# Optimization experiments

Hardware: AMD Instinct MI355X
Metric: run time of the kernel (lower is better)

## Reference

```python
import jax, jax.numpy as jnp
import numpy as np

SOFTCAP = 15.0
EPS_RMS = 1e-6
EPS_L2 = 1e-12


def rms_norm(x):
    # F.rms_norm without affine weight
    return x * jax.lax.rsqrt(jnp.mean(x * x, axis=-1, keepdims=True) + EPS_RMS)


def l2_normalize(x):
    # F.normalize(dim=-1): x / max(||x||, eps)
    n = jnp.sqrt(jnp.sum(x * x, axis=-1, keepdims=True))
    return x / jnp.maximum(n, EPS_L2)


def setup_inputs() -> dict:
    key = jax.random.key(0)
    ks = jax.random.split(key, 7)
    B, D, H, KVH, HD = 2, 1024, 16, 4, 64
    chunk_start_idx, chunk_len, n_scratchpad = 2048, 2048, 64
    T = chunk_start_idx + chunk_len + n_scratchpad  # 4160
    s = 0.02
    return {
        "x": jax.random.normal(ks[0], (B, T, D), dtype=jnp.float32),
        "Wq": jax.random.normal(ks[1], (D, D), dtype=jnp.float32) * s,
        "Wk": jax.random.normal(ks[2], (KVH * HD, D), dtype=jnp.float32) * s,
        "Wv": jax.random.normal(ks[3], (KVH * HD, D), dtype=jnp.float32) * s,
        "Wo": jax.random.normal(ks[4], (D, D), dtype=jnp.float32) * s,
        "Wfc": jax.random.normal(ks[5], (4 * D, D), dtype=jnp.float32) * s,
        "Wproj": jax.random.normal(ks[6], (D, 4 * D), dtype=jnp.float32) * s,
        "chunk_start_idx": chunk_start_idx,
        "chunk_len": chunk_len,
        "n_scratchpad": n_scratchpad,
    }


def reference(x, Wq, Wk, Wv, Wo, Wfc, Wproj, chunk_start_idx, chunk_len, n_scratchpad):
    B, T, D = x.shape
    H = 16
    KVH = Wk.shape[0] // (D // H)
    HD = D // H
    update_start = chunk_start_idx
    n_update = T - update_start

    x_norm = rms_norm(x)
    x_upd = x_norm[:, update_start:]

    q = (x_upd @ Wq.T).reshape(B, n_update, H, HD).transpose(0, 2, 1, 3)   # [B,H,Q,hd]
    k = (x_norm @ Wk.T).reshape(B, T, KVH, HD).transpose(0, 2, 1, 3)       # [B,KVH,T,hd]
    v = (x_norm @ Wv.T).reshape(B, T, KVH, HD).transpose(0, 2, 1, 3)

    q = l2_normalize(q)
    k = l2_normalize(k)

    if KVH < H:
        rep = H // KVH
        k = jnp.repeat(k, rep, axis=1)
        v = jnp.repeat(v, rep, axis=1)

    scale = 1.0 / jnp.sqrt(jnp.float32(HD))
    scores = jnp.einsum("bhqd,bhkd->bhqk", q, k) * scale
    q_pos = jnp.arange(update_start, T)[:, None]
    kv_pos = jnp.arange(T)[None, :]
    mask = kv_pos <= q_pos  # [Q,T] causal
    scores = jnp.where(mask[None, None], scores, -jnp.inf)
    probs = jax.nn.softmax(scores, axis=-1)
    attn = jnp.einsum("bhqk,bhkd->bhqd", probs, v)             # [B,H,Q,hd]
    attn = attn.transpose(0, 2, 1, 3).reshape(B, n_update, D)

    attn_out = attn @ Wo.T
    attn_out = SOFTCAP * jnp.tanh(attn_out / SOFTCAP)

    x_new = x[:, update_start:] + attn_out
    h = rms_norm(x_new) @ Wfc.T
    h = jnp.square(jax.nn.relu(h))  # nanochat MLP: relu(x)^2
    x_new = x_new + h @ Wproj.T

    if update_start > 0:
        return jnp.concatenate([x[:, :update_start], x_new], axis=1)
    return x_new
```

## Files before the change

kernel.cpp:

```cpp
#include <hip/hip_runtime.h>
#include <hip/hip_bf16.h>

#define B_   2
#define T_   4160
#define D_   1024
#define H_   16
#define KVH_ 4
#define HD_  64
#define UPD  2048
#define NU   2112
#define MQ   (B_*NU)
#define MT   (B_*T_)

typedef unsigned short u16;
typedef unsigned int u32;
typedef __attribute__((ext_vector_type(8))) short bf16x8;
typedef __attribute__((ext_vector_type(4))) float f32x4;
typedef __attribute__((ext_vector_type(4))) unsigned short u16x4;

__device__ __forceinline__ float bf2f(u16 u){ return __uint_as_float(((unsigned)u)<<16); }
__device__ __forceinline__ u16 f2bf(float f){
  unsigned u = __float_as_uint(f);
  u += 0x7FFF + ((u>>16)&1);
  return (u16)(u>>16);
}

__device__ __forceinline__ void gll16(const void* g, void* l){
  __builtin_amdgcn_global_load_lds((const __attribute__((address_space(1))) char*)g,
                                   (__attribute__((address_space(3))) char*)l, 16, 0, 0);
}

__global__ void cast_bf16(const float* __restrict__ in, u16* __restrict__ o, int n){
  int i = blockIdx.x*blockDim.x + threadIdx.x;
  if (i*4 < n){
    float4 v = ((const float4*)in)[i];
    u16x4 u; u.x=f2bf(v.x); u.y=f2bf(v.y); u.z=f2bf(v.z); u.w=f2bf(v.w);
    ((u16x4*)o)[i] = u;
  }
}

__global__ void rmsnorm_kernel(const float* __restrict__ in, u16* __restrict__ obf,
                               float* __restrict__ copy_out, int withcopy){
  int row = blockIdx.x;
  int t = threadIdx.x;
  const float* xr = in + (size_t)row*D_;
  float4 v = ((const float4*)xr)[t];
  float ss = v.x*v.x + v.y*v.y + v.z*v.z + v.w*v.w;
  #pragma unroll
  for (int o=32;o;o>>=1) ss += __shfl_xor(ss, o);
  __shared__ float red[4];
  if ((t&63)==0) red[t>>6] = ss;
  __syncthreads();
  float tot = red[0]+red[1]+red[2]+red[3];
  float sc = rsqrtf(tot*(1.0f/D_) + 1e-6f);
  u16x4 o4; o4.x=f2bf(v.x*sc); o4.y=f2bf(v.y*sc); o4.z=f2bf(v.z*sc); o4.w=f2bf(v.w*sc);
  ((u16x4*)(obf + (size_t)row*D_))[t] = o4;
  if (withcopy && (row % T_) < UPD)
    ((float4*)(copy_out + (size_t)row*D_))[t] = v;
}

__global__ void l2norm_kernel(u16* __restrict__ buf, int nvec){
  int vid = blockIdx.x*4 + (threadIdx.x>>6);
  int ln = threadIdx.x & 63;
  if (vid >= nvec) return;
  u16* p = buf + (size_t)vid*64 + ln;
  float x = bf2f(*p);
  float ss = x*x;
  #pragma unroll
  for (int o=32;o;o>>=1) ss += __shfl_xor(ss, o);
  float n = sqrtf(ss);
  n = (n < 1e-12f) ? 1e-12f : n;
  *p = f2bf(x / n);
}

template<int EPI, int AMAP, int BN>
__global__ __launch_bounds__(256) void gemm_bt(
    const u16* __restrict__ A, const u16* __restrict__ Bw, void* __restrict__ C,
    void* __restrict__ aux, int M, int N, int K)
{
  constexpr int MI = (BN==128) ? 4 : 2;
  __shared__ alignas(16) u16 sA[2][4096];
  __shared__ alignas(16) u16 sB[2][BN*32];
  unsigned nwg = gridDim.x*gridDim.y;
  unsigned flat = blockIdx.y*gridDim.x + blockIdx.x;
  unsigned nf = (flat&7)*(nwg>>3) + (flat>>3);
  int m0 = (int)(nf / gridDim.x) * 128;
  int n0 = (int)(nf % gridDim.x) * BN;
  int tid = threadIdx.x;
  int wv = tid>>6, ln = tid&63;
  int wr = (BN==128) ? (wv>>1) : wv;
  int wc = (BN==128) ? (wv&1)  : 0;
  int lr = ln&15, lg = ln>>4;

  auto stage = [&](int bu, int kt){
    #pragma unroll
    for (int c=0;c<2;c++){
      int ci = c*256 + tid;
      int row = ci>>2, colb = (ci&3)*16;
      int arow = m0 + row;
      if (AMAP==1) arow = (arow/NU)*T_ + UPD + (arow%NU);
      const u16* src = A + (size_t)arow*K + kt*32 + (colb>>1);
      gll16(src, (char*)sA[bu] + (c*256 + wv*64)*16);
    }
    #pragma unroll
    for (int c=0;c<BN/64;c++){
      int ci = c*256 + tid;
      int row = ci>>2, colb = (ci&3)*16;
      const u16* src = Bw + (size_t)(n0+row)*K + kt*32 + (colb>>1);
      gll16(src, (char*)sB[bu] + (c*256 + wv*64)*16);
    }
  };

  f32x4 acc[MI][4] = {};
  int nk = K>>5;
  stage(0,0);
  __syncthreads();
  for (int kt=0; kt<nk; ++kt){
    int bu = kt&1;
    if (kt+1<nk) stage(bu^1, kt+1);
    bf16x8 af[MI], bfr[4];
    #pragma unroll
    for (int i=0;i<MI;i++)
      af[i]  = *(const bf16x8*)&sA[bu][(wr*(MI*16) + i*16 + lr)*32 + lg*8];
    #pragma unroll
    for (int j=0;j<4;j++)
      bfr[j] = *(const bf16x8*)&sB[bu][(wc*64 + j*16 + lr)*32 + lg*8];
    #pragma unroll
    for (int i=0;i<MI;i++)
      #pragma unroll
      for (int j=0;j<4;j++)
        acc[i][j] = __builtin_amdgcn_mfma_f32_16x16x32_bf16(af[i], bfr[j], acc[i][j], 0,0,0);
    __syncthreads();
  }
  #pragma unroll
  for (int i=0;i<MI;i++)
    #pragma unroll
    for (int j=0;j<4;j++){
      int grow0 = m0 + wr*(MI*16) + i*16 + lg*4;
      int gcol  = n0 + wc*64 + j*16 + lr;
      if (EPI==5){
        if (gcol < 256){
          #pragma unroll
          for (int r=0;r<4;r++)
            ((u16*)C)[(size_t)(grow0+r)*256 + gcol] = f2bf(acc[i][j][r]);
        } else {
          int bb = grow0 / T_;
          int t  = grow0 - bb*T_;
          int kvh = (gcol>>6)&3, d = gcol&63;
          u16x4 pk;
          #pragma unroll
          for (int r=0;r<4;r++) pk[r] = f2bf(acc[i][j][r]);
          *(u16x4*)((u16*)aux + ((size_t)((bb*KVH_+kvh)*64 + d))*T_ + t) = pk;
        }
      } else {
        #pragma unroll
        for (int r=0;r<4;r++){
          int grow = grow0 + r;
          float cv = acc[i][j][r];
          if (EPI==0){
            ((u16*)C)[(size_t)grow*N + gcol] = f2bf(cv);
          } else if (EPI==1){
            int b = grow/NU, t = grow - b*NU;
            float e = __expf(cv*(2.0f/15.0f));
            float val = 15.f*(e-1.f)/(e+1.f) + ((const float*)aux)[((size_t)(b*T_ + UPD + t))*D_ + gcol];
            ((float*)C)[(size_t)grow*N + gcol] = val;
          } else if (EPI==2){
            float rr = cv>0.f ? cv : 0.f;
            ((u16*)C)[(size_t)grow*N + gcol] = f2bf(rr*rr);
          } else {
            int b = grow/NU, t = grow - b*NU;
            float val = ((const float*)aux)[(size_t)grow*N + gcol] + cv;
            ((float*)C)[((size_t)(b*T_ + UPD + t))*D_ + gcol] = val;
          }
        }
      }
    }
}

template<bool DIAG>
__device__ __forceinline__ void sm_pack(const f32x4 (&s)[2][4], char* spw,
                                        int lr, int lg, int ktb, int qbg){
  #pragma unroll
  for (int qi=0;qi<2;qi++)
    #pragma unroll
    for (int k2=0;k2<4;k2++){
      float p[4];
      #pragma unroll
      for (int r=0;r<4;r++){
        float pv = __builtin_amdgcn_exp2f(s[qi][k2][r]*0.18033688f);
        if (DIAG){
          int kpos = ktb + k2*16 + lg*4 + r;
          int qpos = qbg + qi*16 + lr;
          if (kpos > qpos) pv = 0.f;
        }
        p[r] = pv;
      }
      __hip_bfloat162 w0 = __float22bfloat162_rn(float2{p[0],p[1]});
      __hip_bfloat162 w1 = __float22bfloat162_rn(float2{p[2],p[3]});
      uint2 wd; wd.x = *(u32*)&w0; wd.y = *(u32*)&w1;
      *(uint2*)(spw + (qi*16+lr)*128 + ((k2*32 + lg*8) ^ ((lr&7)<<4))) = wd;
    }
}

__global__ __launch_bounds__(256) void attn_kernel(
    const u16* __restrict__ qb, const u16* __restrict__ kb,
    const u16* __restrict__ vT, u16* __restrict__ ab)
{
  __shared__ alignas(16) u16 sK[2][64*64];
  __shared__ alignas(16) u16 sV[2][64*64];
  __shared__ alignas(16) u16 sP[4][32*64];
  unsigned flat = (blockIdx.z*4u + blockIdx.y)*66u + blockIdx.x;
  unsigned nf = (flat&7)*66u + (flat>>3);
  int qi_blk = 65 - (int)(nf % 66u);
  unsigned khb = nf / 66u;
  int kh = (int)(khb & 3), b = (int)(khb >> 2);
  int tid = threadIdx.x, wv = tid>>6, ln = tid&63;
  int lr = ln&15, lg = ln>>4;
  int h = kh*4 + wv;
  int qrow0 = qi_blk*32;
  int qbg = UPD + qrow0;
  char* spw = (char*)&sP[wv][0];

  bf16x8 qf[2][2];
  #pragma unroll
  for (int qi=0;qi<2;qi++){
    const u16* qp = qb + (size_t)(b*NU + qrow0 + qi*16 + lr)*D_ + h*HD_;
    qf[qi][0] = *(const bf16x8*)(qp + lg*8);
    qf[qi][1] = *(const bf16x8*)(qp + 32 + lg*8);
  }
  bf16x8 ones;
  #pragma unroll
  for (int i=0;i<8;i++) ones[i] = (short)0x3F80;

  f32x4 accO[2][4] = {};
  f32x4 accD[2] = {};

  auto stage = [&](int bu, int kt){
    #pragma unroll
    for (int cc=0; cc<2; ++cc){
      int ci = cc*256 + tid;
      int row = ci>>3, slotb = (ci&7)*16;
      int scolb = slotb ^ ((row&7)<<4);
      gll16(kb + (size_t)(b*T_ + kt*64 + row)*256 + kh*HD_ + (scolb>>1),
            (char*)sK[bu] + (cc*256 + wv*64)*16);
    }
    #pragma unroll
    for (int cc=0; cc<2; ++cc){
      int ci = cc*256 + tid;
      int row = ci>>3, slotb = (ci&7)*16;
      int scolb = slotb ^ ((row&7)<<4);
      gll16(vT + (size_t)((b*KVH_+kh)*64 + row)*T_ + kt*64 + (scolb>>1),
            (char*)sV[bu] + (cc*256 + wv*64)*16);
    }
  };

  int nkt = 33 + (qi_blk>>1);
  stage(0,0);
  __syncthreads();
  for (int kt=0; kt<nkt; ++kt){
    int bu = kt&1;
    if (kt+1 < nkt) stage(bu^1, kt+1);
    f32x4 s[2][4];
    #pragma unroll
    for (int qi=0;qi<2;qi++)
      #pragma unroll
      for (int k2=0;k2<4;k2++) s[qi][k2] = (f32x4){0.f,0.f,0.f,0.f};
    #pragma unroll
    for (int k2=0;k2<4;k2++){
      int row = k2*16 + lr;
      int sw = (row&7)<<4;
      bf16x8 k0 = *(const bf16x8*)((const char*)sK[bu] + row*128 + ((lg*16)^sw));
      bf16x8 k1 = *(const bf16x8*)((const char*)sK[bu] + row*128 + ((64+lg*16)^sw));
      #pragma unroll
      for (int qi=0;qi<2;qi++){
        s[qi][k2] = __builtin_amdgcn_mfma_f32_16x16x32_bf16(k0, qf[qi][0], s[qi][k2], 0,0,0);
        s[qi][k2] = __builtin_amdgcn_mfma_f32_16x16x32_bf16(k1, qf[qi][1], s[qi][k2], 0,0,0);
      }
    }
    if (kt+1 < nkt) sm_pack<false>(s, spw, lr, lg, kt*64, qbg);
    else            sm_pack<true >(s, spw, lr, lg, kt*64, qbg);
    bf16x8 pf[2][2];
    #pragma unroll
    for (int qi=0;qi<2;qi++)
      #pragma unroll
      for (int hf=0;hf<2;hf++)
        pf[qi][hf] = *(const bf16x8*)(spw + (qi*16+lr)*128 + ((hf*64 + lg*16) ^ ((lr&7)<<4)));
    #pragma unroll
    for (int dt=0; dt<4; ++dt){
      int row = dt*16 + lr;
      int sw = (row&7)<<4;
      bf16x8 v0 = *(const bf16x8*)((const char*)sV[bu] + row*128 + ((lg*16)^sw));
      bf16x8 v1 = *(const bf16x8*)((const char*)sV[bu] + row*128 + ((64+lg*16)^sw));
      #pragma unroll
      for (int qi=0;qi<2;qi++){
        accO[qi][dt] = __builtin_amdgcn_mfma_f32_16x16x32_bf16(pf[qi][0], v0, accO[qi][dt], 0,0,0);
        accO[qi][dt] = __builtin_amdgcn_mfma_f32_16x16x32_bf16(pf[qi][1], v1, accO[qi][dt], 0,0,0);
      }
    }
    #pragma unroll
    for (int qi=0;qi<2;qi++){
      accD[qi] = __builtin_amdgcn_mfma_f32_16x16x32_bf16(pf[qi][0], ones, accD[qi], 0,0,0);
      accD[qi] = __builtin_amdgcn_mfma_f32_16x16x32_bf16(pf[qi][1], ones, accD[qi], 0,0,0);
    }
    __syncthreads();
  }
  #pragma unroll
  for (int qi=0;qi<2;qi++)
    #pragma unroll
    for (int dt=0; dt<4; ++dt)
      #pragma unroll
      for (int r=0;r<4;r++){
        float val = accO[qi][dt][r] / accD[qi][r];
        size_t row = (size_t)(b*NU + qrow0 + qi*16 + lg*4 + r);
        ab[row*D_ + h*HD_ + dt*16 + lr] = f2bf(val);
      }
}

extern "C" void kernel_launch(void* const* d_in, const int* in_sizes, int n_in,
                              void* d_out, int out_size, void* d_ws, size_t ws_size,
                              hipStream_t stream)
{
  const float* x     = (const float*)d_in[0];
  const float* Wq    = (const float*)d_in[1];
  const float* Wk    = (const float*)d_in[2];
  const float* Wv    = (const float*)d_in[3];
  const float* Wo    = (const float*)d_in[4];
  const float* Wfc   = (const float*)d_in[5];
  const float* Wproj = (const float*)d_in[6];
  float* out = (float*)d_out;

  char* ws = (char*)d_ws;
  size_t off = 0;
  auto alloc = [&](size_t bytes)->char*{ char* p = ws + off; off += (bytes + 255) & ~(size_t)255; return p; };
  u16* wqb  = (u16*)alloc((size_t)D_*D_*2);
  u16* wkvb = (u16*)alloc((size_t)512*D_*2);
  u16* wob  = (u16*)alloc((size_t)D_*D_*2);
  u16* wfcb = (u16*)alloc((size_t)4096*D_*2);
  u16* wpb  = (u16*)alloc((size_t)D_*4096*2);
  u16* xn   = (u16*)alloc((size_t)MT*D_*2);
  u16* qB   = (u16*)alloc((size_t)MQ*D_*2);
  u16* kB   = (u16*)alloc((size_t)MT*256*2);
  u16* vTb  = (u16*)alloc((size_t)B_*KVH_*64*T_*2);
  u16* aB   = (u16*)alloc((size_t)MQ*D_*2);
  float* xnew = (float*)alloc((size_t)MQ*D_*4);
  u16* xn2  = (u16*)alloc((size_t)MQ*D_*2);
  u16* hB   = (u16*)alloc((size_t)MQ*4096*2);
  (void)ws_size; (void)in_sizes; (void)n_in; (void)out_size;

  cast_bf16<<<1024, 256, 0, stream>>>(Wq, wqb, D_*D_);
  cast_bf16<<<256,  256, 0, stream>>>(Wk, wkvb, 256*D_);
  cast_bf16<<<256,  256, 0, stream>>>(Wv, wkvb + (size_t)256*D_, 256*D_);
  cast_bf16<<<1024, 256, 0, stream>>>(Wo, wob, D_*D_);
  cast_bf16<<<4096, 256, 0, stream>>>(Wfc, wfcb, 4096*D_);
  cast_bf16<<<4096, 256, 0, stream>>>(Wproj, wpb, D_*4096);

  rmsnorm_kernel<<<MT, 256, 0, stream>>>(x, xn, out, 1);

  gemm_bt<0,1,64><<<dim3(16,33), 256, 0, stream>>>(xn, wqb, qB, nullptr, MQ, D_,  D_);
  gemm_bt<5,0,64><<<dim3(8,65),  256, 0, stream>>>(xn, wkvb, kB, vTb, MT, 512, D_);

  l2norm_kernel<<<(MQ*H_)/4, 256, 0, stream>>>(qB, MQ*H_);
  l2norm_kernel<<<(MT*KVH_)/4, 256, 0, stream>>>(kB, MT*KVH_);

  attn_kernel<<<dim3(66,4,2), 256, 0, stream>>>(qB, kB, vTb, aB);

  gemm_bt<1,0,64><<<dim3(16,33), 256, 0, stream>>>(aB, wob, xnew, (void*)x, MQ, D_, D_);

  rmsnorm_kernel<<<MQ, 256, 0, stream>>>(xnew, xn2, nullptr, 0);
  gemm_bt<2,0,128><<<dim3(32,33), 256, 0, stream>>>(xn2, wfcb, hB, nullptr, MQ, 4096, D_);
  gemm_bt<3,0,64><<<dim3(16,33), 256, 0, stream>>>(hB, wpb, out, xnew, MQ, D_, 4096);
}
```

Baseline: 445.2 us.

## Triple-buffer GEMM and attention loads with vmcnt waits, fuse weight casts

GEMM and attention kernels move from double to triple-buffered LDS staging. Each iteration waits on a partial vmcnt and issues one barrier instead of a full __syncthreads, so loads two tiles ahead overlap compute. Load addresses are precomputed, and the GEMM LDS layout gets an XOR swizzle to reduce bank conflicts. The six weight casts become one launch, and the softmax scale folds into the K l2norm, dropping a multiply in the attention exp. The costs are more LDS per block, which may lower occupancy, and relying on hand-placed waitcnt counts for correctness.

Measured after the change: 454.6 us. 2.1% more time.

```diff
diff --git a/kernel.cpp b/kernel.cpp
--- a/kernel.cpp
+++ b/kernel.cpp
@@ -30,13 +30,29 @@
                                    (__attribute__((address_space(3))) char*)l, 16, 0, 0);
 }
 
-__global__ void cast_bf16(const float* __restrict__ in, u16* __restrict__ o, int n){
-  int i = blockIdx.x*blockDim.x + threadIdx.x;
-  if (i*4 < n){
-    float4 v = ((const float4*)in)[i];
-    u16x4 u; u.x=f2bf(v.x); u.y=f2bf(v.y); u.z=f2bf(v.z); u.w=f2bf(v.w);
-    ((u16x4*)o)[i] = u;
-  }
+template<int N> __device__ __forceinline__ void wait_vm(){
+  if constexpr(N==0) asm volatile("s_waitcnt vmcnt(0)" ::: "memory");
+  else if constexpr(N==3) asm volatile("s_waitcnt vmcnt(3)" ::: "memory");
+  else if constexpr(N==4) asm volatile("s_waitcnt vmcnt(4)" ::: "memory");
+}
+
+__global__ void cast_all(const float* __restrict__ s0, const float* __restrict__ s1,
+                         const float* __restrict__ s2, const float* __restrict__ s3,
+                         const float* __restrict__ s4, const float* __restrict__ s5,
+                         u16* __restrict__ d0, u16* __restrict__ d1, u16* __restrict__ d2,
+                         u16* __restrict__ d3, u16* __restrict__ d4, u16* __restrict__ d5){
+  int blk = blockIdx.x;
+  const float* s; u16* d; int base;
+  if      (blk < 1024){ s=s0; d=d0; base=blk; }
+  else if (blk < 1280){ s=s1; d=d1; base=blk-1024; }
+  else if (blk < 1536){ s=s2; d=d2; base=blk-1280; }
+  else if (blk < 2560){ s=s3; d=d3; base=blk-1536; }
+  else if (blk < 6656){ s=s4; d=d4; base=blk-2560; }
+  else                { s=s5; d=d5; base=blk-6656; }
+  int i = base*256 + threadIdx.x;
+  float4 v = ((const float4*)s)[i];
+  u16x4 u; u.x=f2bf(v.x); u.y=f2bf(v.y); u.z=f2bf(v.z); u.w=f2bf(v.w);
+  ((u16x4*)d)[i] = u;
 }
 
 __global__ void rmsnorm_kernel(const float* __restrict__ in, u16* __restrict__ obf,
@@ -59,7 +75,7 @@
     ((float4*)(copy_out + (size_t)row*D_))[t] = v;
 }
 
-__global__ void l2norm_kernel(u16* __restrict__ buf, int nvec){
+__global__ void l2norm_kernel(u16* __restrict__ buf, int nvec, float scale){
   int vid = blockIdx.x*4 + (threadIdx.x>>6);
   int ln = threadIdx.x & 63;
   if (vid >= nvec) return;
@@ -70,7 +86,7 @@
   for (int o=32;o;o>>=1) ss += __shfl_xor(ss, o);
   float n = sqrtf(ss);
   n = (n < 1e-12f) ? 1e-12f : n;
-  *p = f2bf(x / n);
+  *p = f2bf(x * scale / n);
 }
 
 template<int EPI, int AMAP, int BN>
@@ -79,8 +95,9 @@
     void* __restrict__ aux, int M, int N, int K)
 {
   constexpr int MI = (BN==128) ? 4 : 2;
-  __shared__ alignas(16) u16 sA[2][4096];
-  __shared__ alignas(16) u16 sB[2][BN*32];
+  constexpr int NB = BN/64;
+  __shared__ alignas(16) u16 sA[3][4096];
+  __shared__ alignas(16) u16 sB[3][BN*32];
   unsigned nwg = gridDim.x*gridDim.y;
   unsigned flat = blockIdx.y*gridDim.x + blockIdx.x;
   unsigned nf = (flat&7)*(nwg>>3) + (flat>>3);
@@ -92,45 +109,57 @@
   int wc = (BN==128) ? (wv&1)  : 0;
   int lr = ln&15, lg = ln>>4;
 
+  const char* pA[2]; int dA[2];
+  #pragma unroll
+  for (int c=0;c<2;c++){
+    int ci = c*256 + tid;
+    int row = ci>>2, csw = (ci&3) ^ (row&3);
+    int arow = m0 + row;
+    if (AMAP==1) arow = (arow/NU)*T_ + UPD + (arow%NU);
+    pA[c] = (const char*)A + ((size_t)arow*K + csw*8)*2;
+    dA[c] = (c*256 + wv*64)*16;
+  }
+  const char* pB[NB]; int dB[NB];
+  #pragma unroll
+  for (int c=0;c<NB;c++){
+    int ci = c*256 + tid;
+    int row = ci>>2, csw = (ci&3) ^ (row&3);
+    pB[c] = (const char*)Bw + ((size_t)(n0+row)*K + csw*8)*2;
+    dB[c] = (c*256 + wv*64)*16;
+  }
+
   auto stage = [&](int bu, int kt){
     #pragma unroll
-    for (int c=0;c<2;c++){
-      int ci = c*256 + tid;
-      int row = ci>>2, colb = (ci&3)*16;
-      int arow = m0 + row;
-      if (AMAP==1) arow = (arow/NU)*T_ + UPD + (arow%NU);
-      const u16* src = A + (size_t)arow*K + kt*32 + (colb>>1);
-      gll16(src, (char*)sA[bu] + (c*256 + wv*64)*16);
-    }
-    #pragma unroll
-    for (int c=0;c<BN/64;c++){
-      int ci = c*256 + tid;
-      int row = ci>>2, colb = (ci&3)*16;
-      const u16* src = Bw + (size_t)(n0+row)*K + kt*32 + (colb>>1);
-      gll16(src, (char*)sB[bu] + (c*256 + wv*64)*16);
-    }
+    for (int c=0;c<2;c++)  gll16(pA[c] + kt*64, (char*)sA[bu] + dA[c]);
+    #pragma unroll
+    for (int c=0;c<NB;c++) gll16(pB[c] + kt*64, (char*)sB[bu] + dB[c]);
   };
 
   f32x4 acc[MI][4] = {};
   int nk = K>>5;
-  stage(0,0);
-  __syncthreads();
-  for (int kt=0; kt<nk; ++kt){
-    int bu = kt&1;
-    if (kt+1<nk) stage(bu^1, kt+1);
+  stage(0,0); stage(1,1);
+  for (int t=0; t<nk; ++t){
+    int bu = t%3;
+    if (t+1<nk) wait_vm<2+NB>(); else wait_vm<0>();
+    __builtin_amdgcn_s_barrier();
+    __builtin_amdgcn_sched_barrier(0);
+    if (t+2<nk) stage((t+2)%3, t+2);
     bf16x8 af[MI], bfr[4];
     #pragma unroll
-    for (int i=0;i<MI;i++)
-      af[i]  = *(const bf16x8*)&sA[bu][(wr*(MI*16) + i*16 + lr)*32 + lg*8];
-    #pragma unroll
-    for (int j=0;j<4;j++)
-      bfr[j] = *(const bf16x8*)&sB[bu][(wc*64 + j*16 + lr)*32 + lg*8];
+    for (int i=0;i<MI;i++){
+      int row = wr*(MI*16) + i*16 + lr;
+      af[i] = *(const bf16x8*)&sA[bu][row*32 + (lg ^ (lr&3))*8];
+    }
+    #pragma unroll
+    for (int j=0;j<4;j++){
+      int row = wc*64 + j*16 + lr;
+      bfr[j] = *(const bf16x8*)&sB[bu][row*32 + (lg ^ (lr&3))*8];
+    }
     #pragma unroll
     for (int i=0;i<MI;i++)
       #pragma unroll
       for (int j=0;j<4;j++)
         acc[i][j] = __builtin_amdgcn_mfma_f32_16x16x32_bf16(af[i], bfr[j], acc[i][j], 0,0,0);
-    __syncthreads();
   }
   #pragma unroll
   for (int i=0;i<MI;i++)
@@ -187,7 +216,7 @@
       float p[4];
       #pragma unroll
       for (int r=0;r<4;r++){
-        float pv = __builtin_amdgcn_exp2f(s[qi][k2][r]*0.18033688f);
+        float pv = __builtin_amdgcn_exp2f(s[qi][k2][r]);
         if (DIAG){
           int kpos = ktb + k2*16 + lg*4 + r;
           int qpos = qbg + qi*16 + lr;
@@ -206,8 +235,8 @@
     const u16* __restrict__ qb, const u16* __restrict__ kb,
     const u16* __restrict__ vT, u16* __restrict__ ab)
 {
-  __shared__ alignas(16) u16 sK[2][64*64];
-  __shared__ alignas(16) u16 sV[2][64*64];
+  __shared__ alignas(16) u16 sK[3][64*64];
+  __shared__ alignas(16) u16 sV[3][64*64];
   __shared__ alignas(16) u16 sP[4][32*64];
   unsigned flat = (blockIdx.z*4u + blockIdx.y)*66u + blockIdx.x;
   unsigned nf = (flat&7)*66u + (flat>>3);
@@ -235,31 +264,33 @@
   f32x4 accO[2][4] = {};
   f32x4 accD[2] = {};
 
+  const char* pK[2]; const char* pV[2]; int dst[2];
+  #pragma unroll
+  for (int cc=0; cc<2; ++cc){
+    int ci = cc*256 + tid;
+    int row = ci>>3, slotb = (ci&7)*16;
+    int scolb = slotb ^ ((row&7)<<4);
+    pK[cc] = (const char*)kb + ((size_t)(b*T_ + row)*256 + kh*HD_)*2 + scolb;
+    pV[cc] = (const char*)vT + ((size_t)((b*KVH_+kh)*64 + row)*T_)*2 + scolb;
+    dst[cc] = (cc*256 + wv*64)*16;
+  }
   auto stage = [&](int bu, int kt){
     #pragma unroll
-    for (int cc=0; cc<2; ++cc){
-      int ci = cc*256 + tid;
-      int row = ci>>3, slotb = (ci&7)*16;
-      int scolb = slotb ^ ((row&7)<<4);
-      gll16(kb + (size_t)(b*T_ + kt*64 + row)*256 + kh*HD_ + (scolb>>1),
-            (char*)sK[bu] + (cc*256 + wv*64)*16);
-    }
-    #pragma unroll
-    for (int cc=0; cc<2; ++cc){
-      int ci = cc*256 + tid;
-      int row = ci>>3, slotb = (ci&7)*16;
-      int scolb = slotb ^ ((row&7)<<4);
-      gll16(vT + (size_t)((b*KVH_+kh)*64 + row)*T_ + kt*64 + (scolb>>1),
-            (char*)sV[bu] + (cc*256 + wv*64)*16);
-    }
+    for (int cc=0; cc<2; ++cc)
+      gll16(pK[cc] + kt*32768, (char*)sK[bu] + dst[cc]);
+    #pragma unroll
+    for (int cc=0; cc<2; ++cc)
+      gll16(pV[cc] + kt*128,   (char*)sV[bu] + dst[cc]);
   };
 
   int nkt = 33 + (qi_blk>>1);
-  stage(0,0);
-  __syncthreads();
+  stage(0,0); stage(1,1);
   for (int kt=0; kt<nkt; ++kt){
-    int bu = kt&1;
-    if (kt+1 < nkt) stage(bu^1, kt+1);
+    int bu = kt%3;
+    if (kt+1<nkt) wait_vm<4>(); else wait_vm<0>();
+    __builtin_amdgcn_s_barrier();
+    __builtin_amdgcn_sched_barrier(0);
+    if (kt+2<nkt) stage((kt+2)%3, kt+2);
     f32x4 s[2][4];
     #pragma unroll
     for (int qi=0;qi<2;qi++)
@@ -302,7 +333,6 @@
       accD[qi] = __builtin_amdgcn_mfma_f32_16x16x32_bf16(pf[qi][0], ones, accD[qi], 0,0,0);
       accD[qi] = __builtin_amdgcn_mfma_f32_16x16x32_bf16(pf[qi][1], ones, accD[qi], 0,0,0);
     }
-    __syncthreads();
   }
   #pragma unroll
   for (int qi=0;qi<2;qi++)
@@ -347,20 +377,16 @@
   u16* hB   = (u16*)alloc((size_t)MQ*4096*2);
   (void)ws_size; (void)in_sizes; (void)n_in; (void)out_size;
 
-  cast_bf16<<<1024, 256, 0, stream>>>(Wq, wqb, D_*D_);
-  cast_bf16<<<256,  256, 0, stream>>>(Wk, wkvb, 256*D_);
-  cast_bf16<<<256,  256, 0, stream>>>(Wv, wkvb + (size_t)256*D_, 256*D_);
-  cast_bf16<<<1024, 256, 0, stream>>>(Wo, wob, D_*D_);
-  cast_bf16<<<4096, 256, 0, stream>>>(Wfc, wfcb, 4096*D_);
-  cast_bf16<<<4096, 256, 0, stream>>>(Wproj, wpb, D_*4096);
+  cast_all<<<10752, 256, 0, stream>>>(Wq, Wk, Wv, Wo, Wfc, Wproj,
+                                      wqb, wkvb, wkvb + (size_t)256*D_, wob, wfcb, wpb);
 
   rmsnorm_kernel<<<MT, 256, 0, stream>>>(x, xn, out, 1);
 
   gemm_bt<0,1,64><<<dim3(16,33), 256, 0, stream>>>(xn, wqb, qB, nullptr, MQ, D_,  D_);
   gemm_bt<5,0,64><<<dim3(8,65),  256, 0, stream>>>(xn, wkvb, kB, vTb, MT, 512, D_);
 
-  l2norm_kernel<<<(MQ*H_)/4, 256, 0, stream>>>(qB, MQ*H_);
-  l2norm_kernel<<<(MT*KVH_)/4, 256, 0, stream>>>(kB, MT*KVH_);
+  l2norm_kernel<<<(MQ*H_)/4, 256, 0, stream>>>(qB, MQ*H_, 1.0f);
+  l2norm_kernel<<<(MT*KVH_)/4, 256, 0, stream>>>(kB, MT*KVH_, 0.18033688f);
 
   attn_kernel<<<dim3(66,4,2), 256, 0, stream>>>(qB, kB, vTb, aB);
 
```
